# Kernel tuning notes

Hardware: AMD Instinct MI355X
Metric: run time of the kernel (lower is better)

The kernel has to match this reference:

```python
import jax, jax.numpy as jnp
import numpy as np
from jax import lax

EPS = 1e-5

def conv3x3(x, w):
    # NCHW conv, stride 1, padding 1, no bias
    return lax.conv_general_dilated(x, w, window_strides=(1, 1),
                                    padding=((1, 1), (1, 1)),
                                    dimension_numbers=('NCHW', 'OIHW', 'NCHW'))

def bn_train(x, gamma, beta):
    # training-mode BatchNorm2d: batch stats over (N,H,W), biased variance
    mean = jnp.mean(x, axis=(0, 2, 3), keepdims=True)
    var = jnp.mean((x - mean) ** 2, axis=(0, 2, 3), keepdims=True)
    xn = (x - mean) * lax.rsqrt(var + EPS)
    return xn * gamma[None, :, None, None] + beta[None, :, None, None]

def maxpool2(x):
    return lax.reduce_window(x, -jnp.inf, lax.max, (1, 1, 2, 2), (1, 1, 2, 2), 'VALID')

def decomposed_layer(x, dfe_w, dse_g, dse_b, dse_w, bn_g, bn_b):
    # DFE: conv without bias
    x_dfe = conv3x3(x, dfe_w)                     # [B, T, H, W]
    # DSE vectorized: per-channel BN(1)+ReLU == per-channel BN over T, then
    # 1x1 conv 1->G per channel == scalar expand; concat == interleave (i*G+g)
    xr = jax.nn.relu(bn_train(x_dfe, dse_g, dse_b))
    B, T, H, W = xr.shape
    G = dse_w.shape[1]
    x_dse = jnp.einsum('bihw,ig->bighw', xr, dse_w).reshape(B, T * G, H, W)
    # DFE's BN + ReLU
    return jax.nn.relu(bn_train(x_dse, bn_g, bn_b))

def setup_inputs() -> dict:
    key = jax.random.key(0)
    ks = jax.random.split(key, 12)
    B, G = 4096, 2
    d = {}
    d['x'] = jax.random.normal(ks[0], (B, 3, 32, 32), dtype=jnp.float32)
    # layer 1: T_dfe = ceil(16/2) = 8
    d['dfe1_w'] = jax.random.normal(ks[1], (8, 3, 3, 3), dtype=jnp.float32) * 0.1
    d['dse1_g'] = jnp.ones((8,), jnp.float32)
    d['dse1_b'] = jnp.zeros((8,), jnp.float32)
    d['dse1_w'] = jax.random.normal(ks[2], (8, G), dtype=jnp.float32) * 0.3
    d['bn1_g'] = jnp.ones((16,), jnp.float32)
    d['bn1_b'] = jnp.zeros((16,), jnp.float32)
    # layer 2: T_dfe = ceil(32/2) = 16
    d['dfe2_w'] = jax.random.normal(ks[3], (16, 16, 3, 3), dtype=jnp.float32) * 0.1
    d['dse2_g'] = jnp.ones((16,), jnp.float32)
    d['dse2_b'] = jnp.zeros((16,), jnp.float32)
    d['dse2_w'] = jax.random.normal(ks[4], (16, G), dtype=jnp.float32) * 0.3
    d['bn2_g'] = jnp.ones((32,), jnp.float32)
    d['bn2_b'] = jnp.zeros((32,), jnp.float32)
    # FC head
    d['fc1_w'] = jax.random.normal(ks[5], (512, 32 * 8 * 8), dtype=jnp.float32) * 0.02
    d['fc1_b'] = jnp.zeros((512,), jnp.float32)
    d['fc2_w'] = jax.random.normal(ks[6], (512, 512), dtype=jnp.float32) * 0.04
    d['fc2_b'] = jnp.zeros((512,), jnp.float32)
    d['fc3_w'] = jax.random.normal(ks[7], (10, 512), dtype=jnp.float32) * 0.04
    d['fc3_b'] = jnp.zeros((10,), jnp.float32)
    return d

def reference(x, dfe1_w, dse1_g, dse1_b, dse1_w, bn1_g, bn1_b,
              dfe2_w, dse2_g, dse2_b, dse2_w, bn2_g, bn2_b,
              fc1_w, fc1_b, fc2_w, fc2_b, fc3_w, fc3_b):
    h = decomposed_layer(x, dfe1_w, dse1_g, dse1_b, dse1_w, bn1_g, bn1_b)   # [B,16,32,32]
    h = maxpool2(h)                                                          # [B,16,16,16]
    h = decomposed_layer(h, dfe2_w, dse2_g, dse2_b, dse2_w, bn2_g, bn2_b)   # [B,32,16,16]
    h = maxpool2(h)                                                          # [B,32,8,8]
    h = h.reshape(h.shape[0], -1)                                            # [B,2048]
    h = jax.nn.relu(h @ fc1_w.T + fc1_b)
    h = jax.nn.relu(h @ fc2_w.T + fc2_b)
    return h @ fc3_w.T + fc3_b                                               # [B,10]
```

## Files before the change

### kernel.cpp

```cpp
#include <hip/hip_runtime.h>
#include <math.h>

#define EPS_BN 1e-5

namespace {

constexpr double CNT1 = 4096.0 * 1024.0;
constexpr double CNT2 = 4096.0 * 256.0;

constexpr size_t OFF_Y1 = 0;
constexpr size_t OFF_Y2 = 67108864;
constexpr size_t OFF_H2 = 100663296;
constexpr size_t OFF_A1 = 117440512;
constexpr size_t OFF_A2 = 121634816;
constexpr size_t OFF_ST = 134217728;
constexpr size_t OFF_WT = 134234112;
constexpr size_t OFF_WB1 = 134283264;
constexpr size_t OFF_WB2 = 136380416;

#define STG(p, i) (p)[(size_t)(i) * 8]

typedef short bf16x8 __attribute__((ext_vector_type(8)));
typedef float f32x4 __attribute__((ext_vector_type(4)));
typedef _Float16 f16;
typedef _Float16 f16x2 __attribute__((ext_vector_type(2)));
typedef _Float16 f16x4 __attribute__((ext_vector_type(4)));
typedef _Float16 f16x8 __attribute__((ext_vector_type(8)));

__device__ __forceinline__ short f2bf(float f) {
  unsigned u = __float_as_uint(f);
  u = (u + 0x7fffu + ((u >> 16) & 1u)) >> 16;
  return (short)u;
}

__device__ __forceinline__ void block_stats_lds(const float* s, const float* q,
                                                float* __restrict__ sred,
                                                double* __restrict__ st) {
  const int tid = threadIdx.x;
#pragma unroll
  for (int j = 0; j < 8; ++j) {
    sred[j * 257 + tid] = s[j];
    sred[(j + 8) * 257 + tid] = q[j];
  }
  __syncthreads();
  const int row = tid >> 4, seg = tid & 15;
  float p = 0.f;
#pragma unroll
  for (int k = 0; k < 16; ++k) {
    const int ke = (k + seg) & 15;
    p += sred[row * 257 + seg * 16 + ke];
  }
  p += __shfl_down(p, 8, 64);
  p += __shfl_down(p, 4, 64);
  p += __shfl_down(p, 2, 64);
  p += __shfl_down(p, 1, 64);
  if (seg == 0) {
    const int c = (row < 8) ? row : row - 8;
    const int slot = (row < 8) ? 2 * c : 2 * c + 1;
    unsafeAtomicAdd(st + (size_t)slot * 8, (double)p);
  }
}

__device__ __forceinline__ float wave_sum(float v) {
#pragma unroll
  for (int o = 32; o > 0; o >>= 1) v += __shfl_down(v, o, 64);
  return v;
}

__global__ __launch_bounds__(256) void k_conv1_y1(
    const float* __restrict__ x, const float* __restrict__ wt,
    f16* __restrict__ y1, double* __restrict__ st1) {
  __shared__ float sred[16 * 257];
  const int tid = threadIdx.x;
  const int img = tid >> 5, c = tid & 31;
  const int n = blockIdx.x * 8 + img;
  const float* xp = x + (size_t)n * 3072 + c;
  f16* yp = y1 + (size_t)n * 8192;
  float a0[8], a1[8], a2[8], s[8], q[8];
#pragma unroll
  for (int co = 0; co < 8; ++co) {
    a0[co] = 0.f; a1[co] = 0.f; a2[co] = 0.f; s[co] = 0.f; q[co] = 0.f;
  }
  float xM[3];
  xM[0] = xp[0]; xM[1] = xp[1024]; xM[2] = xp[2048];

#define CONTRIB(ACC, T, XV)                                           \
  {                                                                   \
    const float4 wa = *(const float4*)&wt[(T) * 8];                   \
    const float4 wb = *(const float4*)&wt[(T) * 8 + 4];               \
    ACC[0] += wa.x * (XV); ACC[1] += wa.y * (XV);                     \
    ACC[2] += wa.z * (XV); ACC[3] += wa.w * (XV);                     \
    ACC[4] += wb.x * (XV); ACC[5] += wb.y * (XV);                     \
    ACC[6] += wb.z * (XV); ACC[7] += wb.w * (XV);                     \
  }

#define STEP(R, AP, AC, AN)                                           \
  {                                                                   \
    float nM0 = 0.f, nM1 = 0.f, nM2 = 0.f;                            \
    if ((R) <= 30) {                                                  \
      const float* rp = xp + ((R) + 1) * 32;                          \
      nM0 = rp[0]; nM1 = rp[1024]; nM2 = rp[2048];                    \
    }                                                                 \
    _Pragma("unroll") for (int ci = 0; ci < 3; ++ci) {                \
      const float xm = xM[ci];                                        \
      float xl = __shfl_up(xm, 1, 64);                                \
      float xr = __shfl_down(xm, 1, 64);                              \
      if (c == 0) xl = 0.f;                                           \
      if (c == 31) xr = 0.f;                                          \
      CONTRIB(AN, ci * 9 + 0, xl);                                    \
      CONTRIB(AN, ci * 9 + 1, xm);                                    \
      CONTRIB(AN, ci * 9 + 2, xr);                                    \
      CONTRIB(AC, ci * 9 + 3, xl);                                    \
      CONTRIB(AC, ci * 9 + 4, xm);                                    \
      CONTRIB(AC, ci * 9 + 5, xr);                                    \
      CONTRIB(AP, ci * 9 + 6, xl);                                    \
      CONTRIB(AP, ci * 9 + 7, xm);                                    \
      CONTRIB(AP, ci * 9 + 8, xr);                                    \
    }                                                                 \
    if ((R) >= 1) {                                                   \
      f16 hv[8];                                                      \
      _Pragma("unroll") for (int co = 0; co < 8; ++co) {              \
        float v = AP[co];                                             \
        s[co] += v; q[co] += v * v; hv[co] = (f16)v;                  \
      }                                                               \
      *(uint4*)&yp[(size_t)((R) - 1) * 256 + c * 8] = *(uint4*)hv;    \
    }                                                                 \
    _Pragma("unroll") for (int co = 0; co < 8; ++co) AP[co] = 0.f;    \
    xM[0] = nM0; xM[1] = nM1; xM[2] = nM2;                            \
  }

  for (int rb = 0; rb < 33; rb += 3) {
    STEP(rb,     a2, a0, a1);
    STEP(rb + 1, a0, a1, a2);
    STEP(rb + 2, a1, a2, a0);
  }
#undef STEP
#undef CONTRIB
  block_stats_lds(s, q, sred, st1 + (size_t)(blockIdx.x & 7) * 128);
}

__global__ __launch_bounds__(256) void k_xr1_stats(
    const f16* __restrict__ y1, const float* __restrict__ g1,
    const float* __restrict__ b1, const double* __restrict__ st1,
    double* __restrict__ st2) {
  __shared__ float sred[16 * 257];
  __shared__ float sA[8], sC[8];
  if (threadIdx.x < 8) {
    const int c = threadIdx.x;
    double sd = 0.0, qd = 0.0;
#pragma unroll
    for (int b = 0; b < 8; ++b) {
      sd += STG(st1, b * 16 + 2 * c);
      qd += STG(st1, b * 16 + 2 * c + 1);
    }
    double md = sd / CNT1;
    float inv = (float)(1.0 / sqrt(qd / CNT1 - md * md + (double)EPS_BN));
    float a = inv * g1[c];
    sA[c] = a;
    sC[c] = b1[c] - (float)md * a;
  }
  __syncthreads();
  float a1[8], c1[8];
#pragma unroll
  for (int c = 0; c < 8; ++c) { a1[c] = sA[c]; c1[c] = sC[c]; }
  const size_t base = (size_t)blockIdx.x * 4096 + threadIdx.x;
  float s[8], q[8];
#pragma unroll
  for (int c = 0; c < 8; ++c) { s[c] = 0.f; q[c] = 0.f; }
#pragma unroll
  for (int k = 0; k < 16; ++k) {
    f16x8 v = *(const f16x8*)&y1[(base + (size_t)k * 256) * 8];
#pragma unroll
    for (int c = 0; c < 8; ++c) {
      float xr = fmaxf((float)v[c] * a1[c] + c1[c], 0.f);
      s[c] += xr; q[c] += xr * xr;
    }
  }
  block_stats_lds(s, q, sred, st2);
}

__global__ __launch_bounds__(256) void k_conv2_fused(
    const f16* __restrict__ y1, const float* __restrict__ g1,
    const float* __restrict__ b1, const float* __restrict__ dsew,
    const float* __restrict__ bng, const float* __restrict__ bnb,
    const float* __restrict__ w2, const double* __restrict__ st1,
    const double* __restrict__ st2, f16* __restrict__ y2,
    double* __restrict__ st3) {
  __shared__ short smem[4 * 5184 + 10 * 256];
  __shared__ float red[4][32];
  __shared__ float cA1[8], cC1[8], cS2[16], cO2[16];
  short* hs = smem;
  short* wt = smem + 4 * 5184;
  const int tid = threadIdx.x, wid = tid >> 6, lane = tid & 63;
  for (int i = tid; i < (4 * 5184 + 10 * 256) / 2; i += 256) ((int*)smem)[i] = 0;
  if (tid < 16) {
    const int i = tid >> 1, g = tid & 1;
    double sd = 0.0, qd = 0.0;
#pragma unroll
    for (int b = 0; b < 8; ++b) {
      sd += STG(st1, b * 16 + 2 * i);
      qd += STG(st1, b * 16 + 2 * i + 1);
    }
    double md = sd / CNT1;
    float inv1 = (float)(1.0 / sqrt(qd / CNT1 - md * md + (double)EPS_BN));
    float a1 = inv1 * g1[i];
    if (g == 0) { cA1[i] = a1; cC1[i] = b1[i] - (float)md * a1; }
    double s2 = STG(st2, 2 * i), q2 = STG(st2, 2 * i + 1);
    double mx = s2 / CNT1, vx = q2 / CNT1 - mx * mx;
    float w = dsew[i * 2 + g];
    double inv2 = 1.0 / sqrt((double)w * w * vx + (double)EPS_BN);
    cS2[tid] = (float)(w * inv2) * bng[tid];
    cO2[tid] = bnb[tid] - (float)(w * mx * inv2) * bng[tid];
  }
  __syncthreads();
  for (int i = tid; i < 2304; i += 256) {
    const int s = i >> 8, co = (i >> 4) & 15, ci = i & 15;
    wt[i] = f2bf(w2[(co * 16 + ci) * 9 + s]);
  }
  const int c = lane & 15, quad = lane >> 4;
  const int ci0 = (quad & 1) * 8;
  int aoff[5];
#pragma unroll
  for (int p = 0; p < 5; ++p) {
    int s = 2 * p + (quad >> 1);
    if (s > 8) s = 8;
    const int dy = s / 3, dx = s % 3;
    aoff[p] = (dy * 18 + (c + dx)) * 16 + ci0;
  }
  float ssum = 0.f, qsum = 0.f;
  const int n0 = blockIdx.x * 4;
  __syncthreads();
  for (int e = tid; e < 2048; e += 256) {
    const int im = e >> 9, j = e & 511, px = j >> 1, half = j & 1;
    const int r = px >> 4, cx = px & 15;
    const size_t pb =
        ((size_t)(n0 + im) * 1024 + (size_t)(2 * r) * 32 + 2 * cx) * 8 +
        half * 4;
    f16x4 vA = *(const f16x4*)&y1[pb];
    f16x4 vB = *(const f16x4*)&y1[pb + 8];
    f16x4 vC = *(const f16x4*)&y1[pb + 256];
    f16x4 vD = *(const f16x4*)&y1[pb + 264];
    short hv[8];
#pragma unroll
    for (int ii = 0; ii < 4; ++ii) {
      const int i = half * 4 + ii;
      float a = cA1[i], cb = cC1[i];
      float x0 = fmaxf((float)vA[ii] * a + cb, 0.f);
      float x1 = fmaxf((float)vB[ii] * a + cb, 0.f);
      float x2 = fmaxf((float)vC[ii] * a + cb, 0.f);
      float x3 = fmaxf((float)vD[ii] * a + cb, 0.f);
#pragma unroll
      for (int g = 0; g < 2; ++g) {
        const int ch = 2 * i + g;
        float sc = cS2[ch], of = cO2[ch];
        float r0 = fmaxf(x0 * sc + of, 0.f);
        float r1 = fmaxf(x1 * sc + of, 0.f);
        float r2 = fmaxf(x2 * sc + of, 0.f);
        float r3 = fmaxf(x3 * sc + of, 0.f);
        hv[ii * 2 + g] = f2bf(fmaxf(fmaxf(r0, r1), fmaxf(r2, r3)));
      }
    }
    *(uint4*)&hs[im * 5184 + ((r + 1) * 18 + (cx + 1)) * 16 + half * 8] =
        *(uint4*)hv;
  }
  __syncthreads();
  bf16x8 bf[5];
#pragma unroll
  for (int p = 0; p < 5; ++p) {
    const int s = 2 * p + (quad >> 1);
    bf[p] = *(const bf16x8*)&wt[s * 256 + c * 16 + ci0];
  }
  const short* hbase = hs + wid * 5184;
  const int img = n0 + wid;
  f16* yp = y2 + ((size_t)img * 16 + c) * 256 + quad * 4;
  for (int r = 0; r < 16; ++r) {
    f32x4 acc = {0.f, 0.f, 0.f, 0.f};
#pragma unroll
    for (int p = 0; p < 5; ++p) {
      bf16x8 a = *(const bf16x8*)&hbase[r * 288 + aoff[p]];
      acc = __builtin_amdgcn_mfma_f32_16x16x32_bf16(a, bf[p], acc, 0, 0, 0);
    }
    f16 hv[4];
#pragma unroll
    for (int g = 0; g < 4; ++g) {
      hv[g] = (f16)acc[g];
      float v = (float)hv[g];
      ssum += v; qsum += v * v;
    }
    *(f16x4*)&yp[r * 16] = *(f16x4*)hv;
  }
  ssum += __shfl_down(ssum, 32, 64); ssum += __shfl_down(ssum, 16, 64);
  qsum += __shfl_down(qsum, 32, 64); qsum += __shfl_down(qsum, 16, 64);
  if (lane < 16) { red[wid][lane] = ssum; red[wid][16 + lane] = qsum; }
  __syncthreads();
  if (tid < 32) {
    const int cc2 = tid & 15, isq = tid >> 4;
    float v = red[0][isq * 16 + cc2] + red[1][isq * 16 + cc2] +
              red[2][isq * 16 + cc2] + red[3][isq * 16 + cc2];
    unsafeAtomicAdd(st3 + (size_t)(2 * cc2 + isq) * 8, (double)v);
  }
}

__global__ __launch_bounds__(256) void k_xr2_stats(
    const f16* __restrict__ y2, const float* __restrict__ g2,
    const float* __restrict__ b2, const double* __restrict__ st3,
    double* __restrict__ st4) {
  __shared__ float red[32];
  const int tid = threadIdx.x, c = tid >> 4, seg = tid & 15;
  double sd = STG(st3, 2 * c), qd = STG(st3, 2 * c + 1);
  double md = sd / CNT2;
  float inv = (float)(1.0 / sqrt(qd / CNT2 - md * md + (double)EPS_BN));
  float a3 = inv * g2[c];
  float c3 = b2[c] - (float)md * a3;
  float s = 0.f, q = 0.f;
#pragma unroll
  for (int k = 0; k < 8; ++k) {
    const f16* p =
        &y2[(((size_t)(blockIdx.x * 8 + k)) * 16 + c) * 256 + seg * 16];
    f16x8 v0 = *(const f16x8*)p;
    f16x8 v1 = *(const f16x8*)(p + 8);
#pragma unroll
    for (int j = 0; j < 8; ++j) {
      float x0 = fmaxf((float)v0[j] * a3 + c3, 0.f);
      float x1 = fmaxf((float)v1[j] * a3 + c3, 0.f);
      s += x0 + x1; q += x0 * x0 + x1 * x1;
    }
  }
#pragma unroll
  for (int o = 8; o > 0; o >>= 1) {
    s += __shfl_down(s, o, 64);
    q += __shfl_down(q, o, 64);
  }
  if ((tid & 15) == 0) { red[2 * c] = s; red[2 * c + 1] = q; }
  __syncthreads();
  if (tid < 32) unsafeAtomicAdd(st4 + (size_t)tid * 8, (double)red[tid]);
}

__global__ __launch_bounds__(256) void k_l2_out(
    const f16* __restrict__ y2, const float* __restrict__ g2,
    const float* __restrict__ b2, const float* __restrict__ dsew,
    const float* __restrict__ bng, const float* __restrict__ bnb,
    const double* __restrict__ st3, const double* __restrict__ st4,
    short* __restrict__ h2) {
  __shared__ float cS3[16], cO3[16], cS4[32], cO4[32];
  const int tid = threadIdx.x;
  if (tid < 32) {
    const int i = tid >> 1, g = tid & 1;
    double sd = STG(st3, 2 * i), qd = STG(st3, 2 * i + 1);
    double md = sd / CNT2;
    float inv3 = (float)(1.0 / sqrt(qd / CNT2 - md * md + (double)EPS_BN));
    float a3 = inv3 * g2[i];
    if (g == 0) { cS3[i] = a3; cO3[i] = b2[i] - (float)md * a3; }
    double s4 = STG(st4, 2 * i), q4 = STG(st4, 2 * i + 1);
    double mx = s4 / CNT2, vx = q4 / CNT2 - mx * mx;
    float w = dsew[2 * i + g];
    double inv4 = 1.0 / sqrt((double)w * w * vx + (double)EPS_BN);
    cS4[tid] = (float)(w * inv4) * bng[tid];
    cO4[tid] = bnb[tid] - (float)(w * mx * inv4) * bng[tid];
  }
  __syncthreads();
  const int sub = tid >> 6, lane = tid & 63;
  const int n = blockIdx.x * 4 + sub;
  const int px = lane & 7, py = lane >> 3;
#pragma unroll
  for (int i = 0; i < 16; ++i) {
    const size_t base = ((size_t)n * 16 + i) * 256;
    f16x2 v01 = *(const f16x2*)&y2[base + (2 * py) * 16 + 2 * px];
    f16x2 v23 = *(const f16x2*)&y2[base + (2 * py + 1) * 16 + 2 * px];
    float a3 = cS3[i], c3 = cO3[i];
    float xr0 = fmaxf((float)v01[0] * a3 + c3, 0.f);
    float xr1 = fmaxf((float)v01[1] * a3 + c3, 0.f);
    float xr2 = fmaxf((float)v23[0] * a3 + c3, 0.f);
    float xr3 = fmaxf((float)v23[1] * a3 + c3, 0.f);
#pragma unroll
    for (int g = 0; g < 2; ++g) {
      const int c = 2 * i + g;
      float sc = cS4[c], of = cO4[c];
      float r0 = fmaxf(xr0 * sc + of, 0.f);
      float r1 = fmaxf(xr1 * sc + of, 0.f);
      float r2 = fmaxf(xr2 * sc + of, 0.f);
      float r3 = fmaxf(xr3 * sc + of, 0.f);
      h2[(size_t)n * 2048 + c * 64 + py * 8 + px] =
          f2bf(fmaxf(fmaxf(r0, r1), fmaxf(r2, r3)));
    }
  }
}

__global__ __launch_bounds__(256) void k_cast_w(const float* __restrict__ w1,
                                                const float* __restrict__ w2,
                                                const float* __restrict__ dfe1,
                                                short* __restrict__ o1,
                                                short* __restrict__ o2,
                                                double* __restrict__ st,
                                                float* __restrict__ wt) {
  const int i4 = blockIdx.x * 256 + threadIdx.x;
  if (blockIdx.x == 0) {
    for (int k = threadIdx.x; k < 1664; k += 256) st[k] = 0.0;
    if (threadIdx.x < 216)
      wt[(threadIdx.x % 27) * 8 + threadIdx.x / 27] = dfe1[threadIdx.x];
  }
  if (i4 < 262144) {
    float4 v = ((const float4*)w1)[i4];
    short h[4] = {f2bf(v.x), f2bf(v.y), f2bf(v.z), f2bf(v.w)};
    ((uint2*)o1)[i4] = *(uint2*)h;
  } else if (i4 < 327680) {
    const int j = i4 - 262144;
    float4 v = ((const float4*)w2)[j];
    short h[4] = {f2bf(v.x), f2bf(v.y), f2bf(v.z), f2bf(v.w)};
    ((uint2*)o2)[j] = *(uint2*)h;
  }
}

template <int K, int RELU, int OUT_BF16>
__global__ __launch_bounds__(256) void k_fc_lds(
    const short* __restrict__ A, const short* __restrict__ W,
    const float* __restrict__ bias, void* __restrict__ Cv) {
  __shared__ __align__(16) short lds[2][2][64 * 64];
  const int tid = threadIdx.x, w = tid >> 6, lane = tid & 63;
  const int id = blockIdx.y * 8 + blockIdx.x;
  const int bx = (id >> 3) & 7;
  const int by = ((id >> 6) << 3) | (id & 7);
  const int bm = by * 64, bn = bx * 64;
  const int cl = lane & 15, quad = lane >> 4;
  const int srow = lane >> 3, sseg = lane & 7;
  const size_t soff = (size_t)srow * K + ((size_t)(sseg ^ srow) << 3);
  const short* aS0 = A + (size_t)(bm + w * 16) * K + soff;
  const short* aS1 = A + (size_t)(bm + w * 16 + 8) * K + soff;
  const short* bS0 = W + (size_t)(bn + w * 16) * K + soff;
  const short* bS1 = W + (size_t)(bn + w * 16 + 8) * K + soff;

#define GLD16(src, dst)                                                    \
  __builtin_amdgcn_global_load_lds(                                        \
      (const __attribute__((address_space(1))) void*)(const void*)(src),   \
      (__attribute__((address_space(3))) void*)(void*)(dst), 16, 0, 0)
#define STAGE(buf, k0)                                               \
  do {                                                               \
    GLD16(aS0 + (k0), &lds[buf][0][(w * 16) * 64]);                  \
    GLD16(aS1 + (k0), &lds[buf][0][(w * 16 + 8) * 64]);              \
    GLD16(bS0 + (k0), &lds[buf][1][(w * 16) * 64]);                  \
    GLD16(bS1 + (k0), &lds[buf][1][(w * 16 + 8) * 64]);              \
  } while (0)

  f32x4 acc[4];
#pragma unroll
  for (int ct = 0; ct < 4; ++ct) acc[ct] = (f32x4){0.f, 0.f, 0.f, 0.f};
  int aOff[2], bOff0[2];
#pragma unroll
  for (int kk = 0; kk < 2; ++kk) {
    const int sw = ((kk * 4 + quad) ^ (cl & 7)) << 3;
    aOff[kk] = (w * 16 + cl) * 64 + sw;
    bOff0[kk] = cl * 64 + sw;
  }
  constexpr int NT = K / 64;
  STAGE(0, 0);
#pragma unroll 2
  for (int t = 0; t < NT; ++t) {
    asm volatile("s_waitcnt vmcnt(0)" ::: "memory");
    __syncthreads();
    if (t + 1 < NT) STAGE((t + 1) & 1, (t + 1) * 64);
    const short* As = &lds[t & 1][0][0];
    const short* Bs = &lds[t & 1][1][0];
#pragma unroll
    for (int kk = 0; kk < 2; ++kk) {
      bf16x8 a = *(const bf16x8*)&As[aOff[kk]];
#pragma unroll
      for (int ct = 0; ct < 4; ++ct) {
        bf16x8 b = *(const bf16x8*)&Bs[bOff0[kk] + ct * 1024];
        acc[ct] = __builtin_amdgcn_mfma_f32_16x16x32_bf16(a, b, acc[ct], 0, 0, 0);
      }
    }
  }
#undef STAGE
#undef GLD16
#pragma unroll
  for (int ct = 0; ct < 4; ++ct) {
    const int col = bn + ct * 16 + cl;
    const float bia = bias[col];
#pragma unroll
    for (int r = 0; r < 4; ++r) {
      const int row = bm + w * 16 + quad * 4 + r;
      float v = acc[ct][r] + bia;
      if (RELU) v = fmaxf(v, 0.f);
      if (OUT_BF16)
        ((short*)Cv)[(size_t)row * 512 + col] = f2bf(v);
      else
        ((float*)Cv)[(size_t)row * 512 + col] = v;
    }
  }
}

__global__ __launch_bounds__(256) void k_fc3(const float* __restrict__ A,
                                             const float* __restrict__ W,
                                             const float* __restrict__ b,
                                             float* __restrict__ out) {
  const int wid = threadIdx.x >> 6, lane = threadIdx.x & 63;
  const int row = blockIdx.x * 4 + wid;
  float p[10];
#pragma unroll
  for (int o = 0; o < 10; ++o) p[o] = 0.f;
  const float* a = A + (size_t)row * 512;
#pragma unroll
  for (int jj = 0; jj < 8; ++jj) {
    const int j = lane + jj * 64;
    float av = a[j];
#pragma unroll
    for (int o = 0; o < 10; ++o) p[o] += av * W[o * 512 + j];
  }
#pragma unroll
  for (int o = 0; o < 10; ++o) p[o] = wave_sum(p[o]);
  if (lane == 0) {
#pragma unroll
    for (int o = 0; o < 10; ++o) out[(size_t)row * 10 + o] = p[o] + b[o];
  }
}

}

extern "C" void kernel_launch(void* const* d_in, const int* in_sizes, int n_in,
                              void* d_out, int out_size, void* d_ws,
                              size_t ws_size, hipStream_t stream) {
  const float* x      = (const float*)d_in[0];
  const float* dfe1_w = (const float*)d_in[1];
  const float* dse1_g = (const float*)d_in[2];
  const float* dse1_b = (const float*)d_in[3];
  const float* dse1_w = (const float*)d_in[4];
  const float* bn1_g  = (const float*)d_in[5];
  const float* bn1_b  = (const float*)d_in[6];
  const float* dfe2_w = (const float*)d_in[7];
  const float* dse2_g = (const float*)d_in[8];
  const float* dse2_b = (const float*)d_in[9];
  const float* dse2_w = (const float*)d_in[10];
  const float* bn2_g  = (const float*)d_in[11];
  const float* bn2_b  = (const float*)d_in[12];
  const float* fc1_w  = (const float*)d_in[13];
  const float* fc1_b  = (const float*)d_in[14];
  const float* fc2_w  = (const float*)d_in[15];
  const float* fc2_b  = (const float*)d_in[16];
  const float* fc3_w  = (const float*)d_in[17];
  const float* fc3_b  = (const float*)d_in[18];
  float* out = (float*)d_out;
  char* ws = (char*)d_ws;
  f16* y1 = (f16*)(ws + OFF_Y1);
  f16* y2 = (f16*)(ws + OFF_Y2);
  short* h2 = (short*)(ws + OFF_H2);
  short* a1 = (short*)(ws + OFF_A1);
  float* a2 = (float*)(ws + OFF_A2);
  short* wb1 = (short*)(ws + OFF_WB1);
  short* wb2 = (short*)(ws + OFF_WB2);
  float* wt1 = (float*)(ws + OFF_WT);
  double* st = (double*)(ws + OFF_ST);
  double* ST1 = st;
  double* ST2 = st + (size_t)128 * 8;
  double* ST3 = st + (size_t)144 * 8;
  double* ST4 = st + (size_t)176 * 8;

  k_cast_w<<<1280, 256, 0, stream>>>(fc1_w, fc2_w, dfe1_w, wb1, wb2, st, wt1);
  k_conv1_y1<<<512, 256, 0, stream>>>(x, wt1, y1, ST1);
  k_xr1_stats<<<1024, 256, 0, stream>>>(y1, dse1_g, dse1_b, ST1, ST2);
  k_conv2_fused<<<1024, 256, 0, stream>>>(y1, dse1_g, dse1_b, dse1_w, bn1_g,
                                          bn1_b, dfe2_w, ST1, ST2, y2, ST3);
  k_xr2_stats<<<512, 256, 0, stream>>>(y2, dse2_g, dse2_b, ST3, ST4);
  k_l2_out<<<1024, 256, 0, stream>>>(y2, dse2_g, dse2_b, dse2_w, bn2_g, bn2_b,
                                     ST3, ST4, h2);
  k_fc_lds<2048, 1, 1><<<dim3(8, 64), 256, 0, stream>>>(h2, wb1, fc1_b, a1);
  k_fc_lds<512, 1, 0><<<dim3(8, 64), 256, 0, stream>>>(a1, wb2, fc2_b, a2);
  k_fc3<<<1024, 256, 0, stream>>>(a2, fc3_w, fc3_b, out);
}
```

Measured before the change: 296.7 us.

## Split conv1 output channels across waves and keep weights in registers

Each block of conv1 now covers 2 images, and each of its 4 waves computes 2 of the 8 output channels, so the grid grows fourfold and each thread needs far fewer accumulators. The 54 weights each thread needs are loaded into registers once, instead of being reloaded as float4 pairs on every tap. The aim is more parallelism and less register pressure and weight-load traffic. In exchange, every wave re-reads the same input values (4x redundant x loads), and y1 writes shrink to 4-byte stores scattered within each pixel's 16-byte slot. The block statistics reduction is rewritten for the new thread layout.

New measurement: 285.9 us. 3.7% less time.

```diff
diff --git a/kernel.cpp b/kernel.cpp
--- a/kernel.cpp
+++ b/kernel.cpp
@@ -70,28 +70,33 @@
 __global__ __launch_bounds__(256) void k_conv1_y1(
     const float* __restrict__ x, const float* __restrict__ wt,
     f16* __restrict__ y1, double* __restrict__ st1) {
-  __shared__ float sred[16 * 257];
+  __shared__ float sred[16 * 65];
   const int tid = threadIdx.x;
-  const int img = tid >> 5, c = tid & 31;
-  const int n = blockIdx.x * 8 + img;
+  const int g = __builtin_amdgcn_readfirstlane(tid >> 6);
+  const int lane = tid & 63;
+  const int img = lane >> 5, c = lane & 31;
+  const int n = blockIdx.x * 2 + img;
+  const int co0 = 2 * g;
   const float* xp = x + (size_t)n * 3072 + c;
   f16* yp = y1 + (size_t)n * 8192;
-  float a0[8], a1[8], a2[8], s[8], q[8];
-#pragma unroll
-  for (int co = 0; co < 8; ++co) {
-    a0[co] = 0.f; a1[co] = 0.f; a2[co] = 0.f; s[co] = 0.f; q[co] = 0.f;
+  float wA[27], wB[27];
+#pragma unroll
+  for (int t = 0; t < 27; ++t) {
+    wA[t] = wt[t * 8 + co0];
+    wB[t] = wt[t * 8 + co0 + 1];
+  }
+  float a0[2], a1[2], a2[2], s[2], q[2];
+#pragma unroll
+  for (int j = 0; j < 2; ++j) {
+    a0[j] = 0.f; a1[j] = 0.f; a2[j] = 0.f; s[j] = 0.f; q[j] = 0.f;
   }
   float xM[3];
   xM[0] = xp[0]; xM[1] = xp[1024]; xM[2] = xp[2048];
 
 #define CONTRIB(ACC, T, XV)                                           \
   {                                                                   \
-    const float4 wa = *(const float4*)&wt[(T) * 8];                   \
-    const float4 wb = *(const float4*)&wt[(T) * 8 + 4];               \
-    ACC[0] += wa.x * (XV); ACC[1] += wa.y * (XV);                     \
-    ACC[2] += wa.z * (XV); ACC[3] += wa.w * (XV);                     \
-    ACC[4] += wb.x * (XV); ACC[5] += wb.y * (XV);                     \
-    ACC[6] += wb.z * (XV); ACC[7] += wb.w * (XV);                     \
+    ACC[0] += wA[T] * (XV);                                           \
+    ACC[1] += wB[T] * (XV);                                           \
   }
 
 #define STEP(R, AP, AC, AN)                                           \
@@ -118,14 +123,14 @@
       CONTRIB(AP, ci * 9 + 8, xr);                                    \
     }                                                                 \
     if ((R) >= 1) {                                                   \
-      f16 hv[8];                                                      \
-      _Pragma("unroll") for (int co = 0; co < 8; ++co) {              \
-        float v = AP[co];                                             \
-        s[co] += v; q[co] += v * v; hv[co] = (f16)v;                  \
-      }                                                               \
-      *(uint4*)&yp[(size_t)((R) - 1) * 256 + c * 8] = *(uint4*)hv;    \
+      float v0 = AP[0], v1 = AP[1];                                   \
+      s[0] += v0; q[0] += v0 * v0;                                    \
+      s[1] += v1; q[1] += v1 * v1;                                    \
+      f16 hv[2] = {(f16)v0, (f16)v1};                                 \
+      *(unsigned*)&yp[(size_t)((R) - 1) * 256 + c * 8 + co0] =        \
+          *(unsigned*)hv;                                             \
     }                                                                 \
-    _Pragma("unroll") for (int co = 0; co < 8; ++co) AP[co] = 0.f;    \
+    AP[0] = 0.f; AP[1] = 0.f;                                         \
     xM[0] = nM0; xM[1] = nM1; xM[2] = nM2;                            \
   }
 
@@ -136,7 +141,24 @@
   }
 #undef STEP
 #undef CONTRIB
-  block_stats_lds(s, q, sred, st1 + (size_t)(blockIdx.x & 7) * 128);
+  sred[(size_t)co0 * 65 + lane] = s[0];
+  sred[(size_t)(co0 + 1) * 65 + lane] = s[1];
+  sred[(size_t)(8 + co0) * 65 + lane] = q[0];
+  sred[(size_t)(8 + co0 + 1) * 65 + lane] = q[1];
+  __syncthreads();
+  const int row = tid >> 4, seg = tid & 15;
+  float p = sred[row * 65 + seg * 4] + sred[row * 65 + seg * 4 + 1] +
+            sred[row * 65 + seg * 4 + 2] + sred[row * 65 + seg * 4 + 3];
+  p += __shfl_down(p, 8, 64);
+  p += __shfl_down(p, 4, 64);
+  p += __shfl_down(p, 2, 64);
+  p += __shfl_down(p, 1, 64);
+  if (seg == 0) {
+    const int cch = (row < 8) ? row : row - 8;
+    const int slot = (row < 8) ? 2 * cch : 2 * cch + 1;
+    unsafeAtomicAdd(st1 + (size_t)(blockIdx.x & 7) * 128 + (size_t)slot * 8,
+                    (double)p);
+  }
 }
 
 __global__ __launch_bounds__(256) void k_xr1_stats(
@@ -555,7 +577,7 @@
   double* ST4 = st + (size_t)176 * 8;
 
   k_cast_w<<<1280, 256, 0, stream>>>(fc1_w, fc2_w, dfe1_w, wb1, wb2, st, wt1);
-  k_conv1_y1<<<512, 256, 0, stream>>>(x, wt1, y1, ST1);
+  k_conv1_y1<<<2048, 256, 0, stream>>>(x, wt1, y1, ST1);
   k_xr1_stats<<<1024, 256, 0, stream>>>(y1, dse1_g, dse1_b, ST1, ST2);
   k_conv2_fused<<<1024, 256, 0, stream>>>(y1, dse1_g, dse1_b, dse1_w, bn1_g,
                                           bn1_b, dfe2_w, ST1, ST2, y2, ST3);
```
